# Kernel tuning notes

Measured on AMD Instinct MI355X. Metric: run time of the kernel, lower is better.

## Reference

```python
import jax, jax.numpy as jnp
import numpy as np

H = 20          # hidden_size
IN = 2          # GRU input / l1 output dim


def setup_inputs() -> dict:
    key = jax.random.key(0)
    ks = jax.random.split(key, 7)
    B = 32768
    s = 1.0 / np.sqrt(H)  # torch default init scale
    hidden = jax.random.normal(ks[0], (1, B, H), dtype=jnp.float32)
    w_ih = jax.random.uniform(ks[1], (3 * H, IN), jnp.float32, -s, s)
    w_hh = jax.random.uniform(ks[2], (3 * H, H), jnp.float32, -s, s)
    b_ih = jax.random.uniform(ks[3], (3 * H,), jnp.float32, -s, s)
    b_hh = jax.random.uniform(ks[4], (3 * H,), jnp.float32, -s, s)
    w_l = jax.random.uniform(ks[5], (IN, H), jnp.float32, -s, s)
    b_l = jax.random.uniform(ks[6], (IN,), jnp.float32, -s, s)
    return {"hidden": hidden, "w_ih": w_ih, "w_hh": w_hh,
            "b_ih": b_ih, "b_hh": b_hh, "w_l": w_l, "b_l": b_l,
            "step": 200}


def reference(hidden, w_ih, w_hh, b_ih, b_hh, w_l, b_l, step):
    reverse = True
    B = hidden.shape[1]
    h0 = hidden[0]                      # [B, H]
    x0 = jnp.zeros((B, IN), hidden.dtype)  # first GRU input is zeros

    def gru_step(carry, _):
        h, x = carry
        gi = x @ w_ih.T + b_ih          # [B, 3H]
        gh = h @ w_hh.T + b_hh          # [B, 3H]
        ir, iz, inn = jnp.split(gi, 3, axis=-1)
        hr, hz, hn = jnp.split(gh, 3, axis=-1)
        r = jax.nn.sigmoid(ir + hr)
        z = jax.nn.sigmoid(iz + hz)
        n = jnp.tanh(inn + r * hn)
        h_new = (1.0 - z) * n + z * h   # [B, H]
        y = h_new @ w_l.T + b_l         # [B, 2] -> next input
        return (h_new, y), y

    (_, _), ys = jax.lax.scan(gru_step, (h0, x0), None, length=step)
    # ys: [step, B, 2]; original appends per-step then reverses the list
    if reverse:
        ys = ys[::-1]
    return jnp.transpose(ys, (1, 0, 2))  # [B, step, 2]
```

## Files before the change

kernel.cpp:

```cpp
#include <hip/hip_runtime.h>

#define HDIM 20
#define BLOCK 256

typedef __fp16 half8 __attribute__((ext_vector_type(8)));
typedef __fp16 half2v __attribute__((ext_vector_type(2)));
typedef float  float4v __attribute__((ext_vector_type(4)));
typedef int    int4v  __attribute__((ext_vector_type(4)));

static __device__ __forceinline__ float4v mfma16(half8 a, half8 b, float4v c) {
    return __builtin_amdgcn_mfma_f32_16x16x32_f16(a, b, c, 0, 0, 0);
}


__global__ __launch_bounds__(BLOCK, 2) void gru_decoder_kernel(
    const float* __restrict__ hidden,
    const float* __restrict__ w_ih,
    const float* __restrict__ w_hh,
    const float* __restrict__ b_ih,
    const float* __restrict__ b_hh,
    const float* __restrict__ w_l,
    const float* __restrict__ b_l,
    const int*  __restrict__ step_ptr,
    float* __restrict__ out,
    int B)
{
    const int tid = threadIdx.x;
    const int l   = tid & 63;
    const int wv  = tid >> 6;
    const int el  = l & 15;
    const int q   = l >> 4;
    const int e   = (blockIdx.x * 4 + wv) * 16 + el;
    const int step = *step_ptr;

    const float NL2E  = -1.4426950408889634f;
    const float T2L2E =  2.8853900817779268f;

    const int u_dst = el >> 2;
    const int g     = el & 3;

    half8 Afold[5], Azero[5], Ay;
    #pragma unroll
    for (int T = 0; T < 5; ++T) {
        const int u  = 4 * T + u_dst;
        const int rr = (g == 0) ? u : (g == 1) ? 20 + u : 40 + u;
        const float sc = (g <= 1) ? NL2E : T2L2E;
        half8 hf, h0;
        #pragma unroll
        for (int j = 0; j < 8; ++j) {
            float af = 0.f, a0 = 0.f;
            if (j < 5) {
                const int uk = 4 * j + q;
                float wx = w_ih[rr * 2 + 0] * w_l[uk] + w_ih[rr * 2 + 1] * w_l[HDIM + uk];
                float wh = w_hh[rr * HDIM + uk];
                if (g <= 1)      { af = wh + wx; a0 = wh; }
                else if (g == 2) { af = wx;      a0 = 0.f; }
                else             { af = wh;      a0 = wh; }
            } else if (j == 7 && q == 0) {
                float bx = w_ih[rr * 2 + 0] * b_l[0] + w_ih[rr * 2 + 1] * b_l[1];
                if (g <= 1)      { af = b_ih[rr] + b_hh[rr] + bx; a0 = b_ih[rr] + b_hh[rr]; }
                else if (g == 2) { af = b_ih[rr] + bx;            a0 = b_ih[rr]; }
                else             { af = b_hh[rr];                 a0 = b_hh[rr]; }
            }
            hf[j] = (__fp16)(af * sc);
            h0[j] = (__fp16)(a0 * sc);
        }
        Afold[T] = hf;
        Azero[T] = h0;
    }
    {
        half8 hy;
        #pragma unroll
        for (int j = 0; j < 8; ++j) {
            float v = 0.f;
            if (el < 2) {
                if (j < 5)                 v = w_l[el * HDIM + 4 * j + q];
                else if (j == 7 && q == 0) v = b_l[el];
            }
            hy[j] = (__fp16)v;
        }
        Ay = hy;
    }

    int w3const;
    {
        half2v c67; c67[0] = (__fp16)0.f; c67[1] = (__fp16)((q == 0) ? 1.f : 0.f);
        w3const = __builtin_bit_cast(int, c67);
    }

    float hprev[5];
    half8 Bf;
    {
        const float* hb = hidden + (size_t)e * HDIM;
        #pragma unroll
        for (int T = 0; T < 5; ++T) hprev[T] = hb[4 * T + q];
        int4v bi;
        bi[0] = __builtin_bit_cast(int, __builtin_amdgcn_cvt_pkrtz(hprev[0], hprev[1]));
        bi[1] = __builtin_bit_cast(int, __builtin_amdgcn_cvt_pkrtz(hprev[2], hprev[3]));
        bi[2] = __builtin_bit_cast(int, __builtin_amdgcn_cvt_pkrtz(hprev[4], 0.f));
        bi[3] = w3const;
        Bf = __builtin_bit_cast(half8, bi);
    }

    const float4v czero = {0.f, 0.f, 0.f, 0.f};

    auto do_step = [&](const half8* A) {
        float4v C[5];
        #pragma unroll
        for (int T = 0; T < 5; ++T) C[T] = mfma16(A[T], Bf, czero);
        #pragma unroll
        for (int T = 0; T < 5; ++T) {
            float r = __builtin_amdgcn_rcpf(1.f + __builtin_amdgcn_exp2f(C[T][0]));
            float z = __builtin_amdgcn_rcpf(1.f + __builtin_amdgcn_exp2f(C[T][1]));
            float npre2 = __builtin_fmaf(r, C[T][3], C[T][2]);
            float tn = __builtin_amdgcn_rcpf(1.f + __builtin_amdgcn_exp2f(npre2));
            float n = __builtin_fmaf(-2.f, tn, 1.f);
            hprev[T] = __builtin_fmaf(z, hprev[T] - n, n);
        }
        int4v bi;
        bi[0] = __builtin_bit_cast(int, __builtin_amdgcn_cvt_pkrtz(hprev[0], hprev[1]));
        bi[1] = __builtin_bit_cast(int, __builtin_amdgcn_cvt_pkrtz(hprev[2], hprev[3]));
        bi[2] = __builtin_bit_cast(int, __builtin_amdgcn_cvt_pkrtz(hprev[4], 0.f));
        bi[3] = w3const;
        Bf = __builtin_bit_cast(half8, bi);
    };

    float* outp = out + (size_t)e * 2 * step;

    do_step(Azero);
    for (int t = 1; t < step; ++t) {
        float4v cy = mfma16(Ay, Bf, czero);
        if (q == 0) {
            float2 st; st.x = cy[0]; st.y = cy[1];
            *(float2*)(outp + 2 * (step - t)) = st;
        }
        do_step(Afold);
    }
    {
        float4v cy = mfma16(Ay, Bf, czero);
        if (q == 0) {
            float2 st; st.x = cy[0]; st.y = cy[1];
            *(float2*)(outp + 0) = st;
        }
    }
}

extern "C" void kernel_launch(void* const* d_in, const int* in_sizes, int n_in,
                              void* d_out, int out_size, void* d_ws, size_t ws_size,
                              hipStream_t stream) {
    const float* hidden = (const float*)d_in[0];
    const float* w_ih   = (const float*)d_in[1];
    const float* w_hh   = (const float*)d_in[2];
    const float* b_ih   = (const float*)d_in[3];
    const float* b_hh   = (const float*)d_in[4];
    const float* w_l    = (const float*)d_in[5];
    const float* b_l    = (const float*)d_in[6];
    const int*   step   = (const int*)d_in[7];
    float* out = (float*)d_out;

    int B = in_sizes[0] / HDIM;
    int grid = B / 64;

    gru_decoder_kernel<<<grid, BLOCK, 0, stream>>>(
        hidden, w_ih, w_hh, b_ih, b_hh, w_l, b_l, step, out, B);
}
```

Baseline: 170.9 us.

## Interleave two independent batch tiles per wave and pair output stores

Each wave now handles two 16-row batch tiles and interleaves their MFMA gate computations and transcendental updates, so one tile's dependent chain can hide the other's latency. The even-step path also unrolls by two and merges two consecutive float2 outputs into one float4 store, deferred by one iteration. The grid is halved and launch bounds loosened, which cuts the number of waves and raises register pressure.

```diff
diff --git a/kernel.cpp b/kernel.cpp
--- a/kernel.cpp
+++ b/kernel.cpp
@@ -13,7 +13,7 @@
 }
 
 
-__global__ __launch_bounds__(BLOCK, 2) void gru_decoder_kernel(
+__global__ __launch_bounds__(BLOCK, 1) void gru_decoder_kernel(
     const float* __restrict__ hidden,
     const float* __restrict__ w_ih,
     const float* __restrict__ w_hh,
@@ -30,7 +30,8 @@
     const int wv  = tid >> 6;
     const int el  = l & 15;
     const int q   = l >> 4;
-    const int e   = (blockIdx.x * 4 + wv) * 16 + el;
+    const int eA  = (blockIdx.x * 4 + wv) * 32 + el;
+    const int eB  = eA + 16;
     const int step = *step_ptr;
 
     const float NL2E  = -1.4426950408889634f;
@@ -88,26 +89,35 @@
         w3const = __builtin_bit_cast(int, c67);
     }
 
-    float hprev[5];
-    half8 Bf;
-    {
-        const float* hb = hidden + (size_t)e * HDIM;
-        #pragma unroll
-        for (int T = 0; T < 5; ++T) hprev[T] = hb[4 * T + q];
+    float hpA[5], hpB[5];
+    half8 BfA, BfB;
+    float4v CA[5], CB[5];
+
+    auto pack_B = [&](const float* hp) -> half8 {
         int4v bi;
-        bi[0] = __builtin_bit_cast(int, __builtin_amdgcn_cvt_pkrtz(hprev[0], hprev[1]));
-        bi[1] = __builtin_bit_cast(int, __builtin_amdgcn_cvt_pkrtz(hprev[2], hprev[3]));
-        bi[2] = __builtin_bit_cast(int, __builtin_amdgcn_cvt_pkrtz(hprev[4], 0.f));
+        bi[0] = __builtin_bit_cast(int, __builtin_amdgcn_cvt_pkrtz(hp[0], hp[1]));
+        bi[1] = __builtin_bit_cast(int, __builtin_amdgcn_cvt_pkrtz(hp[2], hp[3]));
+        bi[2] = __builtin_bit_cast(int, __builtin_amdgcn_cvt_pkrtz(hp[4], 0.f));
         bi[3] = w3const;
-        Bf = __builtin_bit_cast(half8, bi);
+        return __builtin_bit_cast(half8, bi);
+    };
+
+    {
+        const float* hbA = hidden + (size_t)eA * HDIM;
+        const float* hbB = hidden + (size_t)eB * HDIM;
+        #pragma unroll
+        for (int T = 0; T < 5; ++T) { hpA[T] = hbA[4 * T + q]; hpB[T] = hbB[4 * T + q]; }
+        BfA = pack_B(hpA);
+        BfB = pack_B(hpB);
     }
 
     const float4v czero = {0.f, 0.f, 0.f, 0.f};
 
-    auto do_step = [&](const half8* A) {
-        float4v C[5];
+    auto issue_gates = [&](const half8* A, const half8& Bf, float4v* C) {
         #pragma unroll
         for (int T = 0; T < 5; ++T) C[T] = mfma16(A[T], Bf, czero);
+    };
+    auto finish_update = [&](float4v* C, float* hp, half8& Bf) {
         #pragma unroll
         for (int T = 0; T < 5; ++T) {
             float r = __builtin_amdgcn_rcpf(1.f + __builtin_amdgcn_exp2f(C[T][0]));
@@ -115,32 +125,108 @@
             float npre2 = __builtin_fmaf(r, C[T][3], C[T][2]);
             float tn = __builtin_amdgcn_rcpf(1.f + __builtin_amdgcn_exp2f(npre2));
             float n = __builtin_fmaf(-2.f, tn, 1.f);
-            hprev[T] = __builtin_fmaf(z, hprev[T] - n, n);
-        }
-        int4v bi;
-        bi[0] = __builtin_bit_cast(int, __builtin_amdgcn_cvt_pkrtz(hprev[0], hprev[1]));
-        bi[1] = __builtin_bit_cast(int, __builtin_amdgcn_cvt_pkrtz(hprev[2], hprev[3]));
-        bi[2] = __builtin_bit_cast(int, __builtin_amdgcn_cvt_pkrtz(hprev[4], 0.f));
-        bi[3] = w3const;
-        Bf = __builtin_bit_cast(half8, bi);
+            hp[T] = __builtin_fmaf(z, hp[T] - n, n);
+        }
+        Bf = pack_B(hp);
     };
 
-    float* outp = out + (size_t)e * 2 * step;
-
-    do_step(Azero);
-    for (int t = 1; t < step; ++t) {
-        float4v cy = mfma16(Ay, Bf, czero);
-        if (q == 0) {
-            float2 st; st.x = cy[0]; st.y = cy[1];
-            *(float2*)(outp + 2 * (step - t)) = st;
-        }
-        do_step(Afold);
-    }
-    {
-        float4v cy = mfma16(Ay, Bf, czero);
-        if (q == 0) {
-            float2 st; st.x = cy[0]; st.y = cy[1];
-            *(float2*)(outp + 0) = st;
+    float* outA = out + (size_t)eA * 2 * step;
+    float* outB = out + (size_t)eB * 2 * step;
+
+    issue_gates(Azero, BfA, CA);
+    issue_gates(Azero, BfB, CB);
+    finish_update(CA, hpA, BfA);
+    finish_update(CB, hpB, BfB);
+
+    if ((step & 1) || step < 4) {
+        for (int t = 1; t < step; ++t) {
+            issue_gates(Afold, BfA, CA);
+            float4v cyA = mfma16(Ay, BfA, czero);
+            issue_gates(Afold, BfB, CB);
+            float4v cyB = mfma16(Ay, BfB, czero);
+            if (q == 0) {
+                float2 sa; sa.x = cyA[0]; sa.y = cyA[1];
+                *(float2*)(outA + 2 * (step - t)) = sa;
+                float2 sb; sb.x = cyB[0]; sb.y = cyB[1];
+                *(float2*)(outB + 2 * (step - t)) = sb;
+            }
+            finish_update(CA, hpA, BfA);
+            finish_update(CB, hpB, BfB);
+        }
+        float4v cyA = mfma16(Ay, BfA, czero);
+        float4v cyB = mfma16(Ay, BfB, czero);
+        if (q == 0) {
+            float2 sa; sa.x = cyA[0]; sa.y = cyA[1];
+            *(float2*)(outA) = sa;
+            float2 sb; sb.x = cyB[0]; sb.y = cyB[1];
+            *(float2*)(outB) = sb;
+        }
+        return;
+    }
+
+    float4v pendA, pendB;
+    float  *pendpA, *pendpB;
+
+    {
+        issue_gates(Afold, BfA, CA);
+        float4v cyA1 = mfma16(Ay, BfA, czero);
+        issue_gates(Afold, BfB, CB);
+        float4v cyB1 = mfma16(Ay, BfB, czero);
+        finish_update(CA, hpA, BfA);
+        finish_update(CB, hpB, BfB);
+        issue_gates(Afold, BfA, CA);
+        float4v cyA2 = mfma16(Ay, BfA, czero);
+        issue_gates(Afold, BfB, CB);
+        float4v cyB2 = mfma16(Ay, BfB, czero);
+        finish_update(CA, hpA, BfA);
+        finish_update(CB, hpB, BfB);
+        pendA[0] = cyA2[0]; pendA[1] = cyA2[1]; pendA[2] = cyA1[0]; pendA[3] = cyA1[1];
+        pendB[0] = cyB2[0]; pendB[1] = cyB2[1]; pendB[2] = cyB1[0]; pendB[3] = cyB1[1];
+        pendpA = outA + 2 * (step - 2);
+        pendpB = outB + 2 * (step - 2);
+    }
+
+    for (int k = step - 3; k >= 3; k -= 2) {
+        issue_gates(Afold, BfA, CA);
+        float4v cyA1 = mfma16(Ay, BfA, czero);
+        issue_gates(Afold, BfB, CB);
+        float4v cyB1 = mfma16(Ay, BfB, czero);
+        if (q == 0) {
+            *(float4v*)pendpA = pendA;
+            *(float4v*)pendpB = pendB;
+        }
+        finish_update(CA, hpA, BfA);
+        finish_update(CB, hpB, BfB);
+        issue_gates(Afold, BfA, CA);
+        float4v cyA2 = mfma16(Ay, BfA, czero);
+        issue_gates(Afold, BfB, CB);
+        float4v cyB2 = mfma16(Ay, BfB, czero);
+        finish_update(CA, hpA, BfA);
+        finish_update(CB, hpB, BfB);
+        pendA[0] = cyA2[0]; pendA[1] = cyA2[1]; pendA[2] = cyA1[0]; pendA[3] = cyA1[1];
+        pendB[0] = cyB2[0]; pendB[1] = cyB2[1]; pendB[2] = cyB1[0]; pendB[3] = cyB1[1];
+        pendpA = outA + 2 * (k - 1);
+        pendpB = outB + 2 * (k - 1);
+    }
+
+    {
+        issue_gates(Afold, BfA, CA);
+        float4v cyA1 = mfma16(Ay, BfA, czero);
+        issue_gates(Afold, BfB, CB);
+        float4v cyB1 = mfma16(Ay, BfB, czero);
+        if (q == 0) {
+            *(float4v*)pendpA = pendA;
+            *(float4v*)pendpB = pendB;
+        }
+        finish_update(CA, hpA, BfA);
+        finish_update(CB, hpB, BfB);
+        float4v cyA2 = mfma16(Ay, BfA, czero);
+        float4v cyB2 = mfma16(Ay, BfB, czero);
+        if (q == 0) {
+            float4v sa; sa[0] = cyA2[0]; sa[1] = cyA2[1]; sa[2] = cyA1[0]; sa[3] = cyA1[1];
+            *(float4v*)outA = sa;
+            float4v sb; sb[0] = cyB2[0]; sb[1] = cyB2[1]; sb[2] = cyB1[0]; sb[3] = cyB1[1];
+            *(float4v*)outB = sb;
         }
     }
 }
@@ -159,7 +245,7 @@
     float* out = (float*)d_out;
 
     int B = in_sizes[0] / HDIM;
-    int grid = B / 64;
+    int grid = B / 128;
 
     gru_decoder_kernel<<<grid, BLOCK, 0, stream>>>(
         hidden, w_ih, w_hh, b_ih, b_hh, w_l, b_l, step, out, B);
```

New measurement: 190.6 us. 11.5% more time.

## Split each GRU sequence's hidden tiles across two waves with LDS exchange

Applied to the files above, without the earlier changes.

Each group of 16 sequences is now handled by two cooperating wavefronts: one computes 2 of the 5 hidden-unit tiles plus the output projection, the other computes the remaining 3. They exchange packed fp16 hidden state through a double-buffered shared-memory array and synchronize with a block barrier every step. The output projection MFMA is issued inside the step alongside the gate MFMAs. The aim is to shorten the serial per-step dependency chain and raise parallelism, since the grid goes from B/64 to B/16 blocks. The cost is a __syncthreads every timestep and an uneven 2/3 split of work between the two waves.

```diff
diff --git a/kernel.cpp b/kernel.cpp
--- a/kernel.cpp
+++ b/kernel.cpp
@@ -1,7 +1,7 @@
 #include <hip/hip_runtime.h>
 
 #define HDIM 20
-#define BLOCK 256
+#define BLOCK 128
 
 typedef __fp16 half8 __attribute__((ext_vector_type(8)));
 typedef __fp16 half2v __attribute__((ext_vector_type(2)));
@@ -11,37 +11,28 @@
 static __device__ __forceinline__ float4v mfma16(half8 a, half8 b, float4v c) {
     return __builtin_amdgcn_mfma_f32_16x16x32_f16(a, b, c, 0, 0, 0);
 }
-
-
-__global__ __launch_bounds__(BLOCK, 2) void gru_decoder_kernel(
-    const float* __restrict__ hidden,
-    const float* __restrict__ w_ih,
-    const float* __restrict__ w_hh,
-    const float* __restrict__ b_ih,
-    const float* __restrict__ b_hh,
-    const float* __restrict__ w_l,
-    const float* __restrict__ b_l,
-    const int*  __restrict__ step_ptr,
-    float* __restrict__ out,
-    int B)
+static __device__ __forceinline__ int pkrtz(float a, float b) {
+    return __builtin_bit_cast(int, __builtin_amdgcn_cvt_pkrtz(a, b));
+}
+
+
+template<int NT, int T0, bool W0>
+static __device__ __forceinline__ void run_role(
+    const float* __restrict__ w_ih, const float* __restrict__ w_hh,
+    const float* __restrict__ b_ih, const float* __restrict__ b_hh,
+    const float* __restrict__ w_l,  const float* __restrict__ b_l,
+    const float* __restrict__ hb, float* __restrict__ outp,
+    int step, int el, int q, int l, float* xb)
 {
-    const int tid = threadIdx.x;
-    const int l   = tid & 63;
-    const int wv  = tid >> 6;
-    const int el  = l & 15;
-    const int q   = l >> 4;
-    const int e   = (blockIdx.x * 4 + wv) * 16 + el;
-    const int step = *step_ptr;
-
     const float NL2E  = -1.4426950408889634f;
     const float T2L2E =  2.8853900817779268f;
-
     const int u_dst = el >> 2;
     const int g     = el & 3;
 
-    half8 Afold[5], Azero[5], Ay;
+    half8 Afold[NT], Azero[NT], Ay;
     #pragma unroll
-    for (int T = 0; T < 5; ++T) {
+    for (int i = 0; i < NT; ++i) {
+        const int T  = T0 + i;
         const int u  = 4 * T + u_dst;
         const int rr = (g == 0) ? u : (g == 1) ? 20 + u : 40 + u;
         const float sc = (g <= 1) ? NL2E : T2L2E;
@@ -65,10 +56,10 @@
             hf[j] = (__fp16)(af * sc);
             h0[j] = (__fp16)(a0 * sc);
         }
-        Afold[T] = hf;
-        Azero[T] = h0;
-    }
-    {
+        Afold[i] = hf;
+        Azero[i] = h0;
+    }
+    if constexpr (W0) {
         half8 hy;
         #pragma unroll
         for (int j = 0; j < 8; ++j) {
@@ -88,61 +79,114 @@
         w3const = __builtin_bit_cast(int, c67);
     }
 
-    float hprev[5];
+    float hp[NT];
+    #pragma unroll
+    for (int i = 0; i < NT; ++i) hp[i] = hb[4 * (T0 + i) + q];
+
     half8 Bf;
     {
-        const float* hb = hidden + (size_t)e * HDIM;
-        #pragma unroll
-        for (int T = 0; T < 5; ++T) hprev[T] = hb[4 * T + q];
         int4v bi;
-        bi[0] = __builtin_bit_cast(int, __builtin_amdgcn_cvt_pkrtz(hprev[0], hprev[1]));
-        bi[1] = __builtin_bit_cast(int, __builtin_amdgcn_cvt_pkrtz(hprev[2], hprev[3]));
-        bi[2] = __builtin_bit_cast(int, __builtin_amdgcn_cvt_pkrtz(hprev[4], 0.f));
+        bi[0] = pkrtz(hb[q],      hb[4 + q]);
+        bi[1] = pkrtz(hb[8 + q],  hb[12 + q]);
+        bi[2] = pkrtz(hb[16 + q], 0.f);
         bi[3] = w3const;
         Bf = __builtin_bit_cast(half8, bi);
     }
 
     const float4v czero = {0.f, 0.f, 0.f, 0.f};
-
-    auto do_step = [&](const half8* A) {
-        float4v C[5];
-        #pragma unroll
-        for (int T = 0; T < 5; ++T) C[T] = mfma16(A[T], Bf, czero);
-        #pragma unroll
-        for (int T = 0; T < 5; ++T) {
-            float r = __builtin_amdgcn_rcpf(1.f + __builtin_amdgcn_exp2f(C[T][0]));
-            float z = __builtin_amdgcn_rcpf(1.f + __builtin_amdgcn_exp2f(C[T][1]));
-            float npre2 = __builtin_fmaf(r, C[T][3], C[T][2]);
+    int p = 0;
+
+    auto do_step = [&](const half8* A, int ydst, bool do_y) {
+        float4v C[NT];
+        #pragma unroll
+        for (int i = 0; i < NT; ++i) C[i] = mfma16(A[i], Bf, czero);
+        float4v cy = czero;
+        if constexpr (W0) cy = mfma16(Ay, Bf, czero);
+
+        #pragma unroll
+        for (int i = 0; i < NT; ++i) {
+            float r = __builtin_amdgcn_rcpf(1.f + __builtin_amdgcn_exp2f(C[i][0]));
+            float z = __builtin_amdgcn_rcpf(1.f + __builtin_amdgcn_exp2f(C[i][1]));
+            float npre2 = __builtin_fmaf(r, C[i][3], C[i][2]);
             float tn = __builtin_amdgcn_rcpf(1.f + __builtin_amdgcn_exp2f(npre2));
             float n = __builtin_fmaf(-2.f, tn, 1.f);
-            hprev[T] = __builtin_fmaf(z, hprev[T] - n, n);
-        }
+            hp[i] = __builtin_fmaf(z, hp[i] - n, n);
+        }
+
+        int wA = 0, wB = 0;
+        if constexpr (W0) {
+            wA = pkrtz(hp[0], hp[1]);
+            xb[(p * 3 + 0) * 64 + l] = __builtin_bit_cast(float, wA);
+        } else {
+            wA = pkrtz(hp[0], hp[1]);
+            wB = pkrtz(hp[2], 0.f);
+            xb[(p * 3 + 1) * 64 + l] = __builtin_bit_cast(float, wA);
+            xb[(p * 3 + 2) * 64 + l] = __builtin_bit_cast(float, wB);
+        }
+        __syncthreads();
         int4v bi;
-        bi[0] = __builtin_bit_cast(int, __builtin_amdgcn_cvt_pkrtz(hprev[0], hprev[1]));
-        bi[1] = __builtin_bit_cast(int, __builtin_amdgcn_cvt_pkrtz(hprev[2], hprev[3]));
-        bi[2] = __builtin_bit_cast(int, __builtin_amdgcn_cvt_pkrtz(hprev[4], 0.f));
+        if constexpr (W0) {
+            bi[0] = wA;
+            bi[1] = __builtin_bit_cast(int, xb[(p * 3 + 1) * 64 + l]);
+            bi[2] = __builtin_bit_cast(int, xb[(p * 3 + 2) * 64 + l]);
+        } else {
+            bi[0] = __builtin_bit_cast(int, xb[(p * 3 + 0) * 64 + l]);
+            bi[1] = wA;
+            bi[2] = wB;
+        }
         bi[3] = w3const;
         Bf = __builtin_bit_cast(half8, bi);
+        p ^= 1;
+
+        if constexpr (W0) {
+            if (do_y && q == 0) {
+                float2 st; st.x = cy[0]; st.y = cy[1];
+                *(float2*)(outp + 2 * ydst) = st;
+            }
+        }
     };
 
-    float* outp = out + (size_t)e * 2 * step;
-
-    do_step(Azero);
-    for (int t = 1; t < step; ++t) {
+    do_step(Azero, 0, false);
+    for (int t = 1; t < step; ++t)
+        do_step(Afold, step - t, true);
+
+    if constexpr (W0) {
         float4v cy = mfma16(Ay, Bf, czero);
         if (q == 0) {
             float2 st; st.x = cy[0]; st.y = cy[1];
-            *(float2*)(outp + 2 * (step - t)) = st;
-        }
-        do_step(Afold);
-    }
-    {
-        float4v cy = mfma16(Ay, Bf, czero);
-        if (q == 0) {
-            float2 st; st.x = cy[0]; st.y = cy[1];
-            *(float2*)(outp + 0) = st;
-        }
-    }
+            *(float2*)outp = st;
+        }
+    }
+}
+
+__global__ __launch_bounds__(BLOCK, 4) void gru_decoder_kernel(
+    const float* __restrict__ hidden,
+    const float* __restrict__ w_ih,
+    const float* __restrict__ w_hh,
+    const float* __restrict__ b_ih,
+    const float* __restrict__ b_hh,
+    const float* __restrict__ w_l,
+    const float* __restrict__ b_l,
+    const int*  __restrict__ step_ptr,
+    float* __restrict__ out,
+    int B)
+{
+    __shared__ float xbuf[2 * 3 * 64];
+    const int tid = threadIdx.x;
+    const int l   = tid & 63;
+    const int wv  = tid >> 6;
+    const int el  = l & 15;
+    const int q   = l >> 4;
+    const int e   = blockIdx.x * 16 + el;
+    const int step = *step_ptr;
+
+    const float* hb = hidden + (size_t)e * HDIM;
+    float* outp = out + (size_t)e * 2 * step;
+
+    if (wv == 0)
+        run_role<2, 0, true >(w_ih, w_hh, b_ih, b_hh, w_l, b_l, hb, outp, step, el, q, l, xbuf);
+    else
+        run_role<3, 2, false>(w_ih, w_hh, b_ih, b_hh, w_l, b_l, hb, outp, step, el, q, l, xbuf);
 }
 
 extern "C" void kernel_launch(void* const* d_in, const int* in_sizes, int n_in,
@@ -159,7 +203,7 @@
     float* out = (float*)d_out;
 
     int B = in_sizes[0] / HDIM;
-    int grid = B / 64;
+    int grid = B / 16;
 
     gru_decoder_kernel<<<grid, BLOCK, 0, stream>>>(
         hidden, w_ih, w_hh, b_ih, b_hh, w_l, b_l, step, out, B);
```

Result: slower. 178.0 us (+4.2%).
